# Kernel tuning notes

Hardware: AMD Instinct MI355X
Metric: run time of the kernel (lower is better)

## Reference

```python
import jax, jax.numpy as jnp
import numpy as np
import math

D = 256        # embedding_size
NHEAD = 4
HD = D // NHEAD
FF = 2048      # torch TransformerEncoderLayer default dim_feedforward
NLAYER = 3
VOCAB = 30000
OLD = 2048     # resnet50 fc in_features
BPTT = 20
EOS = 2
PAD = 0
MAXLEN = 5000


def make_pe():
    position = np.arange(MAXLEN)[:, None].astype(np.float32)
    div_term = np.exp(np.arange(0, D, 2).astype(np.float32) * (-math.log(10000.0) / D))
    pe = np.zeros((MAXLEN, D), dtype=np.float32)
    pe[:, 0::2] = np.sin(position * div_term)
    pe[:, 1::2] = np.cos(position * div_term)
    return jnp.asarray(pe)  # [maxlen, d]

PE = make_pe()


def setup_inputs() -> dict:
    key = jax.random.key(0)
    ks = jax.random.split(key, 20)
    s = 0.02
    inp = {
        'image_feats': jax.random.normal(ks[0], (64, OLD), jnp.float32),
        'target_ingrs': jax.random.randint(ks[1], (64, BPTT), 0, VOCAB),
        'emb_table': jax.random.normal(ks[2], (VOCAB, D), jnp.float32) * s,
        'W_g2e': jax.random.normal(ks[3], (OLD, D), jnp.float32) * s,
        'b_g2e': jnp.zeros((D,), jnp.float32),
        'W_out': jax.random.normal(ks[4], (D, VOCAB), jnp.float32) * s,
        'b_out': jnp.zeros((VOCAB,), jnp.float32),
    }
    # per-layer transformer params
    Wqkv, bqkv, Wo, bo, W1, b1, W2, b2, g1, be1, g2, be2 = ([] for _ in range(12))
    k = ks[5]
    for l in range(NLAYER):
        k, *sub = jax.random.split(k, 7)
        Wqkv.append(jax.random.normal(sub[0], (D, 3 * D), jnp.float32) * s)
        bqkv.append(jnp.zeros((3 * D,), jnp.float32))
        Wo.append(jax.random.normal(sub[1], (D, D), jnp.float32) * s)
        bo.append(jnp.zeros((D,), jnp.float32))
        W1.append(jax.random.normal(sub[2], (D, FF), jnp.float32) * s)
        b1.append(jnp.zeros((FF,), jnp.float32))
        W2.append(jax.random.normal(sub[3], (FF, D), jnp.float32) * s)
        b2.append(jnp.zeros((D,), jnp.float32))
        g1.append(jnp.ones((D,), jnp.float32)); be1.append(jnp.zeros((D,), jnp.float32))
        g2.append(jnp.ones((D,), jnp.float32)); be2.append(jnp.zeros((D,), jnp.float32))
    stk = lambda xs: jnp.stack(xs)
    inp.update(Wqkv=stk(Wqkv), bqkv=stk(bqkv), Wo=stk(Wo), bo=stk(bo),
               W1=stk(W1), b1=stk(b1), W2=stk(W2), b2=stk(b2),
               g1=stk(g1), be1=stk(be1), g2=stk(g2), be2=stk(be2))
    return inp


def layernorm(x, g, b):
    mu = jnp.mean(x, -1, keepdims=True)
    var = jnp.var(x, -1, keepdims=True)
    return (x - mu) * jax.lax.rsqrt(var + 1e-5) * g + b


def encoder(x, params):
    # x: [S, B, D] (seq-first like torch). Post-norm encoder, ReLU FFN, no mask.
    (Wqkv, bqkv, Wo, bo, W1, b1, W2, b2, g1, be1, g2, be2) = params
    S, B, _ = x.shape
    for l in range(NLAYER):
        qkv = x @ Wqkv[l] + bqkv[l]                  # [S,B,3D]
        q, k, v = jnp.split(qkv, 3, axis=-1)
        def heads(t):  # [S,B,D] -> [B,H,S,hd]
            return t.reshape(S, B, NHEAD, HD).transpose(1, 2, 0, 3)
        q, k, v = heads(q), heads(k), heads(v)
        att = jnp.einsum('bhqd,bhkd->bhqk', q, k) / math.sqrt(HD)
        att = jax.nn.softmax(att, axis=-1)
        o = jnp.einsum('bhqk,bhkd->bhqd', att, v)    # [B,H,S,hd]
        o = o.transpose(2, 0, 1, 3).reshape(S, B, D)
        x = layernorm(x + o @ Wo[l] + bo[l], g1[l], be1[l])
        ff = jax.nn.relu(x @ W1[l] + b1[l]) @ W2[l] + b2[l]
        x = layernorm(x + ff, g2[l], be2[l])
    return x


def mask_from_eos_after(ids):
    # mult_before=False: mask[:,idx] = all(ids[:,1:idx+1] != EOS); mask[:,0]=1
    ne = (ids != EOS)
    ne = ne.at[:, 0].set(True)
    return jnp.cumprod(ne.astype(jnp.int32), axis=1)  # [B,S]


def reference(image_feats, target_ingrs, emb_table, W_g2e, b_g2e, W_out, b_out,
              Wqkv, bqkv, Wo, bo, W1, b1, W2, b2, g1, be1, g2, be2):
    params = (Wqkv, bqkv, Wo, bo, W1, b1, W2, b2, g1, be1, g2, be2)
    B = image_feats.shape[0]
    img_embed = image_feats @ W_g2e + b_g2e          # [B,D]
    bptt = target_ingrs.shape[1]

    # embeds buffer: [bptt, B, D]; position 0 = image embed (note: original code
    # never applies pos_encoder in predict(), so neither do we)
    embeds = jnp.zeros((bptt, B, D), jnp.float32).at[0].set(img_embed)

    probs_steps = []
    words_steps = []
    # loop over decode steps (fixed-length Python loop; each step re-encodes prefix,
    # faithful to original no-KV-cache behavior)
    for i in range(bptt):
        seq = embeds[: i + 1]                        # [i+1, B, D]
        out = encoder(seq, params)[-1]               # [B, D]
        logits = out @ W_out + b_out                 # [B, V]
        sm = jax.nn.softmax(logits, axis=-1)
        widx = jnp.argmax(sm, axis=-1)               # [B]
        probs_steps.append(sm)
        words_steps.append(widx)
        if i + 1 < bptt:
            embeds = embeds.at[i + 1].set(emb_table[widx])

    decoder_out = jnp.stack(probs_steps, axis=1)     # [B, bptt, V]
    sampled_word = jnp.stack(words_steps, axis=1)    # [B, bptt]
    eos = decoder_out[:, :, EOS]
    mask = mask_from_eos_after(target_ingrs)         # [B, bptt] int
    ingr_probs = jnp.max(decoder_out * mask[:, :, None].astype(jnp.float32), axis=1)
    sampled_word = jnp.where(mask == 0, PAD, sampled_word)
    return ingr_probs, sampled_word, eos
```

## Files before the change

kernel.cpp:

```cpp
#include <hip/hip_runtime.h>
#include <math.h>

#define D 256
#define NH 4
#define HDIM 64
#define FFD 2048
#define NL 3
#define VOC 30000
#define BPTT 20
#define BATCH 64
#define NMAX (BPTT*BATCH)
#define NCOLT 118
#define TROWS 32
#define NWG 256
#define NTHR 512

struct Params {
  const float* image_feats; const int* target; const float* emb_table;
  const float* W_g2e; const float* b_g2e;
  const float* W_out; const float* b_out;
  const float* Wqkv; const float* bqkv;
  const float* Wo;   const float* bo;
  const float* W1;   const float* b1;
  const float* W2;   const float* b2;
  const float* g1;   const float* be1;
  const float* g2;   const float* be2;
  float* out_probs; float* out_words; float* out_eos;
  float* embeds; float* xcur; float* xln1; float* qkvb0; float* qkvb;
  float* pp; float* fp; float* logits;
  float* pm; float* pd; float* pv; float* gS;
  int* pi; int* maskS;
  unsigned* flags;
};

__device__ __forceinline__ float cld(const float* p) {
  return __hip_atomic_load(p, __ATOMIC_RELAXED, __HIP_MEMORY_SCOPE_AGENT);
}
__device__ __forceinline__ void cst(float* p, float v) {
  __hip_atomic_store(p, v, __ATOMIC_RELAXED, __HIP_MEMORY_SCOPE_AGENT);
}
__device__ __forceinline__ int cldi(const int* p) {
  return __hip_atomic_load(p, __ATOMIC_RELAXED, __HIP_MEMORY_SCOPE_AGENT);
}
__device__ __forceinline__ void csti(int* p, int v) {
  __hip_atomic_store(p, v, __ATOMIC_RELAXED, __HIP_MEMORY_SCOPE_AGENT);
}

__device__ __forceinline__ float wredsum(float s) {
  for (int off = 32; off; off >>= 1) s += __shfl_down(s, off);
  return __shfl(s, 0);
}
__device__ __forceinline__ float wredmax(float m) {
  for (int off = 32; off; off >>= 1) m = fmaxf(m, __shfl_down(m, off));
  return __shfl(m, 0);
}

__device__ __forceinline__ void gbar(unsigned* flags, unsigned epoch) {
  asm volatile("s_waitcnt vmcnt(0) lgkmcnt(0)" ::: "memory");
  __syncthreads();
  if (threadIdx.x == 0)
    __hip_atomic_store(&flags[(unsigned)blockIdx.x * 32u], epoch,
                       __ATOMIC_RELAXED, __HIP_MEMORY_SCOPE_AGENT);
  int ok;
  do {
    int mine = 1;
    if (threadIdx.x < NWG)
      mine = ((int)(__hip_atomic_load(&flags[(unsigned)threadIdx.x * 32u],
                    __ATOMIC_RELAXED, __HIP_MEMORY_SCOPE_AGENT) - epoch) >= 0);
    ok = __syncthreads_and(mine);
    if (!ok) __builtin_amdgcn_s_sleep(1);
  } while (!ok);
  asm volatile("" ::: "memory");
}

__device__ __forceinline__ void stage32(float (*As)[D], const float* src, long row0) {
  for (int idx = threadIdx.x; idx < TROWS*D; idx += NTHR) {
    int r = idx >> 8, c = idx & 255;
    As[r][c] = cld(src + (row0 + r)*(long)D + c);
  }
}

__device__ __forceinline__ void stageLN(float (*As)[D], const float* resid, long row0,
    const float* parts, int nparts, long pstride,
    const float* bias, const float* g, const float* be, float* wr) {
  const int tid = threadIdx.x;
  for (int idx = tid; idx < TROWS*D; idx += NTHR) {
    int r = idx >> 8, c = idx & 255;
    long row = row0 + r;
    float v = cld(resid + row*D + c) + bias[c];
    for (int q = 0; q < nparts; ++q)
      v += cld(parts + (long)q*pstride + row*D + c);
    As[r][c] = v;
  }
  __syncthreads();
  const int lane = tid & 63, w = tid >> 6;
#pragma unroll
  for (int j = 0; j < 4; ++j) {
    int r = w*4 + j;
    float4 x = *(float4*)&As[r][lane*4];
    float mu = wredsum(x.x+x.y+x.z+x.w) * (1.f/D);
    float dx = x.x-mu, dy = x.y-mu, dz = x.z-mu, dw = x.w-mu;
    float var = wredsum(dx*dx+dy*dy+dz*dz+dw*dw) * (1.f/D);
    float inv = 1.f/sqrtf(var + 1e-5f);
    float4 gg = *(const float4*)&g[lane*4];
    float4 bb = *(const float4*)&be[lane*4];
    float4 o;
    o.x = dx*inv*gg.x + bb.x; o.y = dy*inv*gg.y + bb.y;
    o.z = dz*inv*gg.z + bb.z; o.w = dw*inv*gg.w + bb.w;
    *(float4*)&As[r][lane*4] = o;
    if (wr) {
      long row = row0 + r;
      cst(&wr[row*D + lane*4 + 0], o.x);
      cst(&wr[row*D + lane*4 + 1], o.y);
      cst(&wr[row*D + lane*4 + 2], o.z);
      cst(&wr[row*D + lane*4 + 3], o.w);
    }
  }
  __syncthreads();
}

__device__ __forceinline__ void mm32w(const float (*As)[D], const float* __restrict__ Wp,
                                      long M, float acc[4][4]) {
  const int r0 = (threadIdx.x >> 6) * 4;
  for (int kk = 0; kk < D; kk += 4) {
    float w[4][4];
#pragma unroll
    for (int q = 0; q < 4; ++q)
      *(float4*)w[q] = *(const float4*)(Wp + (long)(kk+q)*M);
#pragma unroll
    for (int j = 0; j < 4; ++j) {
      float a[4];
      *(float4*)a = *(const float4*)&As[r0+j][kk];
#pragma unroll
      for (int c = 0; c < 4; ++c)
#pragma unroll
        for (int q = 0; q < 4; ++q)
          acc[j][c] += a[q]*w[q][c];
    }
  }
}

__global__ __launch_bounds__(NTHR, 2) void mega(Params p) {
  extern __shared__ char smraw[];
  float (*As)[D] = (float(*)[D])smraw;
  float (*Bs)[D] = (float(*)[D])(smraw + TROWS*D*4);
  float* sm = (float*)smraw;
  const int tid = threadIdx.x, wgid = blockIdx.x;
  const int lane = tid & 63, wave = tid >> 6;
  unsigned ep = 0;
  unsigned* flags = p.flags;

  if (wgid < BATCH) {
    int b = wgid;
    for (int idx = tid; idx < 2048; idx += NTHR) sm[idx] = p.image_feats[b*2048 + idx];
    __syncthreads();
    if (tid < D) {
      float acc = 0.f;
      for (int k = 0; k < 2048; k += 4) {
        float4 xv = *(const float4*)&sm[k];
        acc += xv.x * p.W_g2e[(k+0)*D + tid];
        acc += xv.y * p.W_g2e[(k+1)*D + tid];
        acc += xv.z * p.W_g2e[(k+2)*D + tid];
        acc += xv.w * p.W_g2e[(k+3)*D + tid];
      }
      cst(&p.embeds[(long)b*D + tid], acc + p.b_g2e[tid]);
    }
  }
  gbar(flags, ++ep);

  for (int i = 0; i < BPTT; ++i) {
    const int S = i + 1;

    if (wgid >= NCOLT && wgid < NCOLT + 6) {
      int idx = wgid - NCOLT;
      int tt = idx & 1, cp = idx >> 1;
      long row0 = (long)i*BATCH + tt*TROWS;
      stage32(As, p.embeds, row0);
      __syncthreads();
      float acc[4][4] = {};
      int col = cp*256 + lane*4;
      mm32w(As, p.Wqkv + col, 3*D, acc);
      float bv[4]; *(float4*)bv = *(const float4*)(p.bqkv + col);
      const int r0 = wave*4;
      for (int j = 0; j < 4; ++j) {
        long row = row0 + r0 + j;
        for (int c = 0; c < 4; ++c)
          cst(&p.qkvb0[row*768 + col + c], acc[j][c] + bv[c]);
      }
    } else if (wgid < NCOLT && i > 0) {
      float* gm = sm; float* ss = sm + 64; int* mk = (int*)(sm + 128);
      if (tid < 64) {
        gm[tid] = cld(&p.gS[tid*2]); ss[tid] = cld(&p.gS[tid*2+1]);
        mk[tid] = cldi(&p.maskS[tid]);
      }
      __syncthreads();
      int cbase = wgid*256;
      for (int idx = tid; idx < BATCH*256; idx += NTHR) {
        int b = idx >> 8, c = cbase + (idx & 255);
        if (c < VOC && (i-1 == 0 || mk[b])) {
          float l = cld(&p.logits[(long)b*VOC + c]);
          float pr = expf(l - gm[b]) / ss[b];
          float* op = &p.out_probs[(long)b*VOC + c];
          if (i-1 == 0) *op = pr; else *op = fmaxf(*op, pr);
        }
      }
    }
    gbar(flags, ++ep);

    for (int l = 0; l < NL; ++l) {
      {
        const float* src = (l == 0) ? p.qkvb0 : p.qkvb;
        float* qs = sm; float* ks = sm + 1280; float* vs = sm + 2560;
        float* ps = sm + 3840;
        int b = wgid & 63, h = wgid >> 6;
        for (int idx = tid; idx < S*HDIM; idx += NTHR) {
          int s = idx >> 6, d = idx & 63;
          long base = (long)(s*BATCH + b)*768 + h*HDIM + d;
          qs[idx] = cld(&src[base]);
          ks[idx] = cld(&src[base + D]);
          vs[idx] = cld(&src[base + 2*D]);
        }
        __syncthreads();
        const float* Wo2 = p.Wo + (long)l*D*D + (long)h*HDIM*D;
        if (l < NL-1) {
          for (int idx = tid; idx < S*S; idx += NTHR) {
            int si = idx / S, ti = idx - si*S;
            float a = 0.f;
#pragma unroll 8
            for (int k = 0; k < HDIM; ++k) a += qs[si*HDIM+k]*ks[ti*HDIM+k];
            ps[si*(BPTT+1)+ti] = a * 0.125f;
          }
          __syncthreads();
          for (int r = wave; r < S; r += 8) {
            float v = (lane < S) ? ps[r*(BPTT+1)+lane] : -1e30f;
            float m = wredmax(v);
            float e = (lane < S) ? expf(v - m) : 0.f;
            float ssum = wredsum(e);
            if (lane < S) ps[r*(BPTT+1)+lane] = e / ssum;
          }
          __syncthreads();
          for (int idx = tid; idx < S*HDIM; idx += NTHR) {
            int s = idx >> 6, d = idx & 63;
            float a = 0.f;
            for (int t2 = 0; t2 < S; ++t2) a += ps[s*(BPTT+1)+t2]*vs[t2*HDIM+d];
            qs[idx] = a;
          }
          __syncthreads();
          int c0 = lane*4;
          float acc[3][4] = {};
          for (int k = 0; k < HDIM; ++k) {
            float4 w = *(const float4*)&Wo2[(long)k*D + c0];
#pragma unroll
            for (int jj = 0; jj < 3; ++jj) {
              int r = wave + 8*jj;
              float a = (r < S) ? qs[r*HDIM + k] : 0.f;
              acc[jj][0]+=a*w.x; acc[jj][1]+=a*w.y; acc[jj][2]+=a*w.z; acc[jj][3]+=a*w.w;
            }
          }
          for (int jj = 0; jj < 3; ++jj) {
            int r = wave + 8*jj;
            if (r < S) {
              long row = (long)r*BATCH + b;
              for (int c = 0; c < 4; ++c)
                cst(&p.pp[((long)h*NMAX + row)*D + c0 + c], acc[jj][c]);
            }
          }
        } else {
          if (tid < S) {
            float a = 0.f;
            for (int k = 0; k < HDIM; ++k) a += qs[i*HDIM+k]*ks[tid*HDIM+k];
            ps[tid] = a * 0.125f;
          }
          __syncthreads();
          if (wave == 0) {
            float v = (lane < S) ? ps[lane] : -1e30f;
            float m = wredmax(v);
            float e = (lane < S) ? expf(v - m) : 0.f;
            float ssum = wredsum(e);
            if (lane < S) ps[lane] = e / ssum;
          }
          __syncthreads();
          if (tid < HDIM) {
            float a = 0.f;
            for (int t2 = 0; t2 < S; ++t2) a += ps[t2]*vs[t2*HDIM+tid];
            qs[tid] = a;
          }
          __syncthreads();
          if (tid < D) {
            float a = 0.f;
            for (int k = 0; k < HDIM; ++k) a += qs[k]*Wo2[(long)k*D + tid];
            cst(&p.pp[((long)h*NMAX + (long)i*BATCH + b)*D + tid], a);
          }
        }
      }
      gbar(flags, ++ep);

      {
        const float* resid = (l == 0) ? p.embeds : p.xcur;
        const float* bol = p.bo + l*D;
        const float* g1l = p.g1 + l*D; const float* be1l = p.be1 + l*D;
        const float* W1l = p.W1 + (long)l*D*FFD;
        const float* b1l = p.b1 + (long)l*FFD;
        const float* W2l = p.W2 + (long)l*FFD*D;
        const int y = wgid & 7, slot = wgid >> 3;
        const int nrt = (l == NL-1) ? 2 : 2*S;
        const long rbase = (l == NL-1) ? (long)i*BATCH : 0;
        for (int tt = slot; tt < nrt; tt += 32) {
          long row0 = rbase + (long)tt*TROWS;
          stageLN(As, resid, row0, p.pp, 4, (long)NMAX*D, bol, g1l, be1l,
                  (y == 0) ? p.xln1 : nullptr);
          float acc1[4][4] = {};
          int fcol = y*256 + lane*4;
          mm32w(As, W1l + fcol, FFD, acc1);
          float bv[4]; *(float4*)bv = *(const float4*)(b1l + fcol);
          const int r0 = wave*4;
          for (int j = 0; j < 4; ++j)
            for (int c = 0; c < 4; ++c)
              Bs[r0+j][lane*4+c] = fmaxf(acc1[j][c] + bv[c], 0.f);
          __syncthreads();
          float acc2[4][4] = {};
          mm32w(Bs, W2l + (long)(y*256)*D + lane*4, D, acc2);
          for (int j = 0; j < 4; ++j) {
            long row = row0 + r0 + j;
            for (int c = 0; c < 4; ++c)
              cst(&p.fp[((long)y*NMAX + row)*D + lane*4 + c], acc2[j][c]);
          }
          __syncthreads();
        }
      }
      gbar(flags, ++ep);

      if (l + 1 < NL) {
        const float* b2l = p.b2 + l*D;
        const float* g2l = p.g2 + l*D; const float* be2l = p.be2 + l*D;
        const float* Wl = p.Wqkv + (long)(l+1)*D*768;
        const float* bl = p.bqkv + (long)(l+1)*768;
        for (int t = wgid; t < 6*S; t += NWG) {
          int tt = t % (2*S), cp = t / (2*S);
          long row0 = (long)tt*TROWS;
          stageLN(As, p.xln1, row0, p.fp, 8, (long)NMAX*D, b2l, g2l, be2l,
                  (cp == 0) ? p.xcur : nullptr);
          float acc[4][4] = {};
          int col = cp*256 + lane*4;
          mm32w(As, Wl + col, 768, acc);
          float bv[4]; *(float4*)bv = *(const float4*)(bl + col);
          const int r0 = wave*4;
          for (int j = 0; j < 4; ++j) {
            long row = row0 + r0 + j;
            for (int c = 0; c < 4; ++c)
              cst(&p.qkvb[row*768 + col + c], acc[j][c] + bv[c]);
          }
          __syncthreads();
        }
        gbar(flags, ++ep);
      }
    }

    {
      const float* b2l = p.b2 + (NL-1)*D;
      const float* g2l = p.g2 + (NL-1)*D; const float* be2l = p.be2 + (NL-1)*D;
      const int x = wgid & 7, slot = wgid >> 3;
      const int rowt = slot & 1, cq = slot >> 1;
      const int colt = cq*8 + x;
      if (cq < 15 && colt < NCOLT) {
        long row0 = (long)i*BATCH + rowt*TROWS;
        stageLN(As, p.xln1, row0, p.fp, 8, (long)NMAX*D, b2l, g2l, be2l, nullptr);
        int col = colt*256 + lane*4;
        int colL = col > VOC-4 ? VOC-4 : col;
        float acc[4][4] = {};
        mm32w(As, p.W_out + colL, VOC, acc);
        float bv[4]; *(float4*)bv = *(const float4*)(p.b_out + colL);
        bool valid = (col < VOC);
        const int r0 = wave*4;
        for (int j = 0; j < 4; ++j) {
          int b = rowt*TROWS + r0 + j;
          float v4[4]; float lm = -1e30f;
          for (int c = 0; c < 4; ++c) {
            v4[c] = acc[j][c] + bv[c];
            if (valid) { cst(&p.logits[(long)b*VOC + col + c], v4[c]); lm = fmaxf(lm, v4[c]); }
          }
          float m = wredmax(lm);
          float ls = 0.f;
          if (valid) for (int c = 0; c < 4; ++c) ls += expf(v4[c] - m);
          for (int off = 32; off; off >>= 1) ls += __shfl_down(ls, off);
          float av = -1e30f; int ai = VOC;
          if (valid) for (int c = 0; c < 4; ++c) if (v4[c] > av) { av = v4[c]; ai = col + c; }
          for (int off = 32; off; off >>= 1) {
            float av2 = __shfl_down(av, off); int ai2 = __shfl_down(ai, off);
            if (av2 > av || (av2 == av && ai2 < ai)) { av = av2; ai = ai2; }
          }
          if (lane == 0) {
            int pidx = colt*64 + b;
            cst(&p.pm[pidx], m); cst(&p.pd[pidx], ls);
            cst(&p.pv[pidx], av); csti(&p.pi[pidx], ai);
          }
        }
      }
    }
    gbar(flags, ++ep);

    if (wgid < BATCH) {
      int b = wgid;
      float* Lm = sm; float* Ld = sm + 128; float* Lv = sm + 256;
      int* Li = (int*)(sm + 384); int* Lei = Li + 128;
      if (tid < NCOLT) {
        Lm[tid] = cld(&p.pm[tid*64 + b]);
        Ld[tid] = cld(&p.pd[tid*64 + b]);
        Lv[tid] = cld(&p.pv[tid*64 + b]);
        Li[tid] = cldi(&p.pi[tid*64 + b]);
      }
      __syncthreads();
      if (tid == 0) {
        float gmax = -1e30f;
        for (int t2 = 0; t2 < NCOLT; ++t2) gmax = fmaxf(gmax, Lm[t2]);
        float Ssum = 0.f;
        for (int t2 = 0; t2 < NCOLT; ++t2) Ssum += Ld[t2] * expf(Lm[t2] - gmax);
        float bvv = -1e30f; int bi = VOC;
        for (int t2 = 0; t2 < NCOLT; ++t2)
          if (Lv[t2] > bvv || (Lv[t2] == bvv && Li[t2] < bi)) { bvv = Lv[t2]; bi = Li[t2]; }
        int run = 1;
        for (int j = 1; j <= i; ++j) if (p.target[b*BPTT + j] == 2) run = 0;
        float p2 = expf(cld(&p.logits[(long)b*VOC + 2]) - gmax) / Ssum;
        p.out_eos[b*BPTT + i] = p2;
        p.out_words[b*BPTT + i] = run ? (float)bi : 0.f;
        cst(&p.gS[b*2], gmax);
        cst(&p.gS[b*2+1], Ssum);
        csti(&p.maskS[b], run);
        Lei[0] = bi;
      }
      __syncthreads();
      if (i + 1 < BPTT && tid < D) {
        int ei = Lei[0];
        cst(&p.embeds[((long)(i+1)*BATCH + b)*D + tid], p.emb_table[(long)ei*D + tid]);
      }
    }
    gbar(flags, ++ep);
  }

  if (wgid < NCOLT) {
    float* gm = sm; float* ss = sm + 64; int* mk = (int*)(sm + 128);
    if (tid < 64) {
      gm[tid] = cld(&p.gS[tid*2]); ss[tid] = cld(&p.gS[tid*2+1]);
      mk[tid] = cldi(&p.maskS[tid]);
    }
    __syncthreads();
    int cbase = wgid*256;
    for (int idx = tid; idx < BATCH*256; idx += NTHR) {
      int b = idx >> 8, c = cbase + (idx & 255);
      if (c < VOC && mk[b]) {
        float l = cld(&p.logits[(long)b*VOC + c]);
        float pr = expf(l - gm[b]) / ss[b];
        float* op = &p.out_probs[(long)b*VOC + c];
        *op = fmaxf(*op, pr);
      }
    }
  }
}

extern "C" void kernel_launch(void* const* d_in, const int* in_sizes, int n_in,
                              void* d_out, int out_size, void* d_ws, size_t ws_size,
                              hipStream_t stream) {
  Params P;
  P.image_feats = (const float*)d_in[0];
  P.target      = (const int*)  d_in[1];
  P.emb_table   = (const float*)d_in[2];
  P.W_g2e       = (const float*)d_in[3];
  P.b_g2e       = (const float*)d_in[4];
  P.W_out       = (const float*)d_in[5];
  P.b_out       = (const float*)d_in[6];
  P.Wqkv        = (const float*)d_in[7];
  P.bqkv        = (const float*)d_in[8];
  P.Wo          = (const float*)d_in[9];
  P.bo          = (const float*)d_in[10];
  P.W1          = (const float*)d_in[11];
  P.b1          = (const float*)d_in[12];
  P.W2          = (const float*)d_in[13];
  P.b2          = (const float*)d_in[14];
  P.g1          = (const float*)d_in[15];
  P.be1         = (const float*)d_in[16];
  P.g2          = (const float*)d_in[17];
  P.be2         = (const float*)d_in[18];

  float* out_probs = (float*)d_out;
  P.out_probs = out_probs;
  P.out_words = out_probs + (long)BATCH*VOC;
  P.out_eos   = P.out_words + BATCH*BPTT;

  char* ws = (char*)d_ws;
  P.embeds = (float*)ws;  ws += sizeof(float)*(long)NMAX*D;
  P.xcur   = (float*)ws;  ws += sizeof(float)*(long)NMAX*D;
  P.xln1   = (float*)ws;  ws += sizeof(float)*(long)NMAX*D;
  P.qkvb0  = (float*)ws;  ws += sizeof(float)*(long)NMAX*3*D;
  P.qkvb   = (float*)ws;  ws += sizeof(float)*(long)NMAX*3*D;
  P.pp     = (float*)ws;  ws += sizeof(float)*(long)4*NMAX*D;
  P.fp     = (float*)ws;  ws += sizeof(float)*(long)8*NMAX*D;
  P.logits = (float*)ws;  ws += sizeof(float)*(long)BATCH*VOC;
  P.pm     = (float*)ws;  ws += sizeof(float)*NCOLT*64;
  P.pd     = (float*)ws;  ws += sizeof(float)*NCOLT*64;
  P.pv     = (float*)ws;  ws += sizeof(float)*NCOLT*64;
  P.gS     = (float*)ws;  ws += sizeof(float)*128;
  P.pi     = (int*)ws;    ws += sizeof(int)*NCOLT*64;
  P.maskS  = (int*)ws;    ws += sizeof(int)*64;
  P.flags  = (unsigned*)ws; ws += sizeof(unsigned)*NWG*32;

  static bool inited = false;
  if (!inited) {
    hipFuncSetAttribute((const void*)mega,
                        hipFuncAttributeMaxDynamicSharedMemorySize, 65536);
    inited = true;
  }

  hipMemsetAsync(P.flags, 0, sizeof(unsigned)*NWG*32, stream);
  void* args[] = { &P };
  hipError_t err = hipLaunchCooperativeKernel((void*)mega, dim3(NWG), dim3(NTHR),
                                              args, 65536, stream);
  if (err != hipSuccess) {
    hipLaunchKernelGGL(mega, dim3(NWG), dim3(NTHR), 65536, stream, P);
  }
}
```

Measured before the change: 10.53 ms.

## Use master-release grid barrier and 64-bit coherent loads/stores

Replaces the all-to-all flag polling grid barrier with a centralized scheme: block 0 polls every block's arrival flag and then publishes a single release flag that the other blocks spin on. This cuts the number of atomic polling loads each barrier generates. Separately, the relaxed agent-scope atomic loads and stores used for cross-block data are widened from 32-bit to 64-bit (float2) accesses, halving the count of coherent memory operations. The centralized barrier adds one extra hop of latency through block 0.

```diff
diff --git a/kernel.cpp b/kernel.cpp
--- a/kernel.cpp
+++ b/kernel.cpp
@@ -45,6 +45,16 @@
 __device__ __forceinline__ void csti(int* p, int v) {
   __hip_atomic_store(p, v, __ATOMIC_RELAXED, __HIP_MEMORY_SCOPE_AGENT);
 }
+__device__ __forceinline__ float2 cld2(const float* p) {
+  unsigned long long u = __hip_atomic_load((const unsigned long long*)p,
+                                           __ATOMIC_RELAXED, __HIP_MEMORY_SCOPE_AGENT);
+  union { unsigned long long u; float2 f; } x; x.u = u; return x.f;
+}
+__device__ __forceinline__ void cst2(float* p, float a, float b) {
+  union { unsigned long long u; float f[2]; } x; x.f[0] = a; x.f[1] = b;
+  __hip_atomic_store((unsigned long long*)p, x.u,
+                     __ATOMIC_RELAXED, __HIP_MEMORY_SCOPE_AGENT);
+}
 
 __device__ __forceinline__ float wredsum(float s) {
   for (int off = 32; off; off >>= 1) s += __shfl_down(s, off);
@@ -56,27 +66,39 @@
 }
 
 __device__ __forceinline__ void gbar(unsigned* flags, unsigned epoch) {
+  unsigned* rel = flags + NWG*32;
   asm volatile("s_waitcnt vmcnt(0) lgkmcnt(0)" ::: "memory");
   __syncthreads();
-  if (threadIdx.x == 0)
-    __hip_atomic_store(&flags[(unsigned)blockIdx.x * 32u], epoch,
-                       __ATOMIC_RELAXED, __HIP_MEMORY_SCOPE_AGENT);
-  int ok;
-  do {
-    int mine = 1;
-    if (threadIdx.x < NWG)
-      mine = ((int)(__hip_atomic_load(&flags[(unsigned)threadIdx.x * 32u],
-                    __ATOMIC_RELAXED, __HIP_MEMORY_SCOPE_AGENT) - epoch) >= 0);
-    ok = __syncthreads_and(mine);
-    if (!ok) __builtin_amdgcn_s_sleep(1);
-  } while (!ok);
+  if (blockIdx.x == 0) {
+    int ok;
+    do {
+      int mine = 1;
+      if (threadIdx.x > 0 && threadIdx.x < NWG)
+        mine = ((int)(__hip_atomic_load(&flags[(unsigned)threadIdx.x * 32u],
+                      __ATOMIC_RELAXED, __HIP_MEMORY_SCOPE_AGENT) - epoch) >= 0);
+      ok = __syncthreads_and(mine);
+      if (!ok) __builtin_amdgcn_s_sleep(1);
+    } while (!ok);
+    if (threadIdx.x == 0)
+      __hip_atomic_store(rel, epoch, __ATOMIC_RELAXED, __HIP_MEMORY_SCOPE_AGENT);
+  } else {
+    if (threadIdx.x == 0) {
+      __hip_atomic_store(&flags[(unsigned)blockIdx.x * 32u], epoch,
+                         __ATOMIC_RELAXED, __HIP_MEMORY_SCOPE_AGENT);
+      while ((int)(__hip_atomic_load(rel, __ATOMIC_RELAXED,
+                   __HIP_MEMORY_SCOPE_AGENT) - epoch) < 0)
+        __builtin_amdgcn_s_sleep(2);
+    }
+    __syncthreads();
+  }
   asm volatile("" ::: "memory");
 }
 
 __device__ __forceinline__ void stage32(float (*As)[D], const float* src, long row0) {
-  for (int idx = threadIdx.x; idx < TROWS*D; idx += NTHR) {
-    int r = idx >> 8, c = idx & 255;
-    As[r][c] = cld(src + (row0 + r)*(long)D + c);
+  for (int idx = threadIdx.x; idx < TROWS*D/2; idx += NTHR) {
+    int r = idx >> 7, c2 = (idx & 127)*2;
+    float2 v = cld2(src + (row0 + r)*(long)D + c2);
+    As[r][c2] = v.x; As[r][c2+1] = v.y;
   }
 }
 
@@ -84,13 +106,16 @@
     const float* parts, int nparts, long pstride,
     const float* bias, const float* g, const float* be, float* wr) {
   const int tid = threadIdx.x;
-  for (int idx = tid; idx < TROWS*D; idx += NTHR) {
-    int r = idx >> 8, c = idx & 255;
+  for (int idx = tid; idx < TROWS*D/2; idx += NTHR) {
+    int r = idx >> 7, c2 = (idx & 127)*2;
     long row = row0 + r;
-    float v = cld(resid + row*D + c) + bias[c];
-    for (int q = 0; q < nparts; ++q)
-      v += cld(parts + (long)q*pstride + row*D + c);
-    As[r][c] = v;
+    float2 v = cld2(resid + row*D + c2);
+    float vx = v.x + bias[c2], vy = v.y + bias[c2+1];
+    for (int q = 0; q < nparts; ++q) {
+      float2 pv = cld2(parts + (long)q*pstride + row*D + c2);
+      vx += pv.x; vy += pv.y;
+    }
+    As[r][c2] = vx; As[r][c2+1] = vy;
   }
   __syncthreads();
   const int lane = tid & 63, w = tid >> 6;
@@ -110,10 +135,8 @@
     *(float4*)&As[r][lane*4] = o;
     if (wr) {
       long row = row0 + r;
-      cst(&wr[row*D + lane*4 + 0], o.x);
-      cst(&wr[row*D + lane*4 + 1], o.y);
-      cst(&wr[row*D + lane*4 + 2], o.z);
-      cst(&wr[row*D + lane*4 + 3], o.w);
+      cst2(&wr[row*D + lane*4],     o.x, o.y);
+      cst2(&wr[row*D + lane*4 + 2], o.z, o.w);
     }
   }
   __syncthreads();
@@ -184,8 +207,8 @@
       const int r0 = wave*4;
       for (int j = 0; j < 4; ++j) {
         long row = row0 + r0 + j;
-        for (int c = 0; c < 4; ++c)
-          cst(&p.qkvb0[row*768 + col + c], acc[j][c] + bv[c]);
+        cst2(&p.qkvb0[row*768 + col],     acc[j][0] + bv[0], acc[j][1] + bv[1]);
+        cst2(&p.qkvb0[row*768 + col + 2], acc[j][2] + bv[2], acc[j][3] + bv[3]);
       }
     } else if (wgid < NCOLT && i > 0) {
       float* gm = sm; float* ss = sm + 64; int* mk = (int*)(sm + 128);
@@ -195,13 +218,15 @@
       }
       __syncthreads();
       int cbase = wgid*256;
-      for (int idx = tid; idx < BATCH*256; idx += NTHR) {
-        int b = idx >> 8, c = cbase + (idx & 255);
+      for (int idx = tid; idx < BATCH*128; idx += NTHR) {
+        int b = idx >> 7, c = cbase + (idx & 127)*2;
         if (c < VOC && (i-1 == 0 || mk[b])) {
-          float l = cld(&p.logits[(long)b*VOC + c]);
-          float pr = expf(l - gm[b]) / ss[b];
+          float2 l = cld2(&p.logits[(long)b*VOC + c]);
+          float pr0 = expf(l.x - gm[b]) / ss[b];
+          float pr1 = expf(l.y - gm[b]) / ss[b];
           float* op = &p.out_probs[(long)b*VOC + c];
-          if (i-1 == 0) *op = pr; else *op = fmaxf(*op, pr);
+          if (i-1 == 0) { op[0] = pr0; op[1] = pr1; }
+          else { op[0] = fmaxf(op[0], pr0); op[1] = fmaxf(op[1], pr1); }
         }
       }
     }
@@ -213,12 +238,15 @@
         float* qs = sm; float* ks = sm + 1280; float* vs = sm + 2560;
         float* ps = sm + 3840;
         int b = wgid & 63, h = wgid >> 6;
-        for (int idx = tid; idx < S*HDIM; idx += NTHR) {
-          int s = idx >> 6, d = idx & 63;
-          long base = (long)(s*BATCH + b)*768 + h*HDIM + d;
-          qs[idx] = cld(&src[base]);
-          ks[idx] = cld(&src[base + D]);
-          vs[idx] = cld(&src[base + 2*D]);
+        for (int idx = tid; idx < S*32; idx += NTHR) {
+          int s = idx >> 5, d2 = (idx & 31)*2;
+          long base = (long)(s*BATCH + b)*768 + h*HDIM + d2;
+          float2 qv = cld2(&src[base]);
+          float2 kv = cld2(&src[base + D]);
+          float2 vv = cld2(&src[base + 2*D]);
+          qs[s*HDIM+d2] = qv.x; qs[s*HDIM+d2+1] = qv.y;
+          ks[s*HDIM+d2] = kv.x; ks[s*HDIM+d2+1] = kv.y;
+          vs[s*HDIM+d2] = vv.x; vs[s*HDIM+d2+1] = vv.y;
         }
         __syncthreads();
         const float* Wo2 = p.Wo + (long)l*D*D + (long)h*HDIM*D;
@@ -261,8 +289,8 @@
             int r = wave + 8*jj;
             if (r < S) {
               long row = (long)r*BATCH + b;
-              for (int c = 0; c < 4; ++c)
-                cst(&p.pp[((long)h*NMAX + row)*D + c0 + c], acc[jj][c]);
+              cst2(&p.pp[((long)h*NMAX + row)*D + c0],     acc[jj][0], acc[jj][1]);
+              cst2(&p.pp[((long)h*NMAX + row)*D + c0 + 2], acc[jj][2], acc[jj][3]);
             }
           }
         } else {
@@ -286,10 +314,14 @@
             qs[tid] = a;
           }
           __syncthreads();
-          if (tid < D) {
-            float a = 0.f;
-            for (int k = 0; k < HDIM; ++k) a += qs[k]*Wo2[(long)k*D + tid];
-            cst(&p.pp[((long)h*NMAX + (long)i*BATCH + b)*D + tid], a);
+          if (tid < 128) {
+            int c2 = tid*2;
+            float a0 = 0.f, a1 = 0.f;
+            for (int k = 0; k < HDIM; ++k) {
+              a0 += qs[k]*Wo2[(long)k*D + c2];
+              a1 += qs[k]*Wo2[(long)k*D + c2 + 1];
+            }
+            cst2(&p.pp[((long)h*NMAX + (long)i*BATCH + b)*D + c2], a0, a1);
           }
         }
       }
@@ -322,8 +354,8 @@
           mm32w(Bs, W2l + (long)(y*256)*D + lane*4, D, acc2);
           for (int j = 0; j < 4; ++j) {
             long row = row0 + r0 + j;
-            for (int c = 0; c < 4; ++c)
-              cst(&p.fp[((long)y*NMAX + row)*D + lane*4 + c], acc2[j][c]);
+            cst2(&p.fp[((long)y*NMAX + row)*D + lane*4],     acc2[j][0], acc2[j][1]);
+            cst2(&p.fp[((long)y*NMAX + row)*D + lane*4 + 2], acc2[j][2], acc2[j][3]);
           }
           __syncthreads();
         }
@@ -347,8 +379,8 @@
           const int r0 = wave*4;
           for (int j = 0; j < 4; ++j) {
             long row = row0 + r0 + j;
-            for (int c = 0; c < 4; ++c)
-              cst(&p.qkvb[row*768 + col + c], acc[j][c] + bv[c]);
+            cst2(&p.qkvb[row*768 + col],     acc[j][0] + bv[0], acc[j][1] + bv[1]);
+            cst2(&p.qkvb[row*768 + col + 2], acc[j][2] + bv[2], acc[j][3] + bv[3]);
           }
           __syncthreads();
         }
@@ -375,9 +407,11 @@
         for (int j = 0; j < 4; ++j) {
           int b = rowt*TROWS + r0 + j;
           float v4[4]; float lm = -1e30f;
-          for (int c = 0; c < 4; ++c) {
-            v4[c] = acc[j][c] + bv[c];
-            if (valid) { cst(&p.logits[(long)b*VOC + col + c], v4[c]); lm = fmaxf(lm, v4[c]); }
+          for (int c = 0; c < 4; ++c) v4[c] = acc[j][c] + bv[c];
+          if (valid) {
+            cst2(&p.logits[(long)b*VOC + col],     v4[0], v4[1]);
+            cst2(&p.logits[(long)b*VOC + col + 2], v4[2], v4[3]);
+            for (int c = 0; c < 4; ++c) lm = fmaxf(lm, v4[c]);
           }
           float m = wredmax(lm);
           float ls = 0.f;
@@ -429,9 +463,11 @@
         Lei[0] = bi;
       }
       __syncthreads();
-      if (i + 1 < BPTT && tid < D) {
+      if (i + 1 < BPTT && tid < 128) {
         int ei = Lei[0];
-        cst(&p.embeds[((long)(i+1)*BATCH + b)*D + tid], p.emb_table[(long)ei*D + tid]);
+        int c2 = tid*2;
+        cst2(&p.embeds[((long)(i+1)*BATCH + b)*D + c2],
+             p.emb_table[(long)ei*D + c2], p.emb_table[(long)ei*D + c2 + 1]);
       }
     }
     gbar(flags, ++ep);
@@ -445,13 +481,15 @@
     }
     __syncthreads();
     int cbase = wgid*256;
-    for (int idx = tid; idx < BATCH*256; idx += NTHR) {
-      int b = idx >> 8, c = cbase + (idx & 255);
+    for (int idx = tid; idx < BATCH*128; idx += NTHR) {
+      int b = idx >> 7, c = cbase + (idx & 127)*2;
       if (c < VOC && mk[b]) {
-        float l = cld(&p.logits[(long)b*VOC + c]);
-        float pr = expf(l - gm[b]) / ss[b];
+        float2 l = cld2(&p.logits[(long)b*VOC + c]);
+        float pr0 = expf(l.x - gm[b]) / ss[b];
+        float pr1 = expf(l.y - gm[b]) / ss[b];
         float* op = &p.out_probs[(long)b*VOC + c];
-        *op = fmaxf(*op, pr);
+        op[0] = fmaxf(op[0], pr0);
+        op[1] = fmaxf(op[1], pr1);
       }
     }
   }
@@ -501,7 +539,7 @@
   P.gS     = (float*)ws;  ws += sizeof(float)*128;
   P.pi     = (int*)ws;    ws += sizeof(int)*NCOLT*64;
   P.maskS  = (int*)ws;    ws += sizeof(int)*64;
-  P.flags  = (unsigned*)ws; ws += sizeof(unsigned)*NWG*32;
+  P.flags  = (unsigned*)ws; ws += sizeof(unsigned)*(NWG*32 + 32);
 
   static bool inited = false;
   if (!inited) {
@@ -510,7 +548,7 @@
     inited = true;
   }
 
-  hipMemsetAsync(P.flags, 0, sizeof(unsigned)*NWG*32, stream);
+  hipMemsetAsync(P.flags, 0, sizeof(unsigned)*(NWG*32 + 32), stream);
   void* args[] = { &P };
   hipError_t err = hipLaunchCooperativeKernel((void*)mega, dim3(NWG), dim3(NTHR),
                                               args, 65536, stream);
```

Measured after the change: 9.580 ms. -9.0%, faster.
